# Kernel tuning notes

Hardware: AMD Instinct MI355X
Metric: run time of the kernel (lower is better)

## Reference

```python
import jax, jax.numpy as jnp
import numpy as np
from jax import lax

V, B, T, H = 8000, 64, 128, 512
EMB_INIT = 0.5 / 128.0  # init_width = 0.5 / embedding_size


def setup_inputs() -> dict:
    key = jax.random.key(0)
    ks = jax.random.split(key, 9)
    return {
        "input_data": jax.random.randint(ks[0], (B, T), 0, V, dtype=jnp.int64),
        "targets": jax.random.randint(ks[1], (B, T), 0, V, dtype=jnp.int64),
        "embedding": jax.random.uniform(ks[2], (V, H), minval=-EMB_INIT, maxval=EMB_INIT, dtype=jnp.float32),
        "W1": jax.random.normal(ks[3], (2 * H, 4 * H), dtype=jnp.float32) * 0.02,
        "b1": jnp.zeros((4 * H,), dtype=jnp.float32),
        "W2": jax.random.normal(ks[4], (2 * H, 4 * H), dtype=jnp.float32) * 0.02,
        "b2": jnp.zeros((4 * H,), dtype=jnp.float32),
        "softmax_w": jax.random.normal(ks[5], (H, V), dtype=jnp.float32) * 0.02,
        "softmax_b": jnp.zeros((V,), dtype=jnp.float32),
    }


def _lstm_step(c, h, x, W, b):
    # BasicLSTMCell with forget_bias=0.0, gate order i, j, f, o
    gates = jnp.concatenate([x, h], axis=-1) @ W + b  # [B, 4H]
    i, j, f, o = jnp.split(gates, 4, axis=-1)
    c_new = c * jax.nn.sigmoid(f) + jax.nn.sigmoid(i) * jnp.tanh(j)
    h_new = jnp.tanh(c_new) * jax.nn.sigmoid(o)
    return c_new, h_new


def reference(input_data, targets, embedding, W1, b1, W2, b2, softmax_w, softmax_b):
    x = embedding[input_data]            # [B, T, H] embedding lookup
    xt = jnp.transpose(x, (1, 0, 2))     # [T, B, H] time-major for scan

    def step(carry, x_t):
        c1, h1, c2, h2 = carry
        c1, h1 = _lstm_step(c1, h1, x_t, W1, b1)
        c2, h2 = _lstm_step(c2, h2, h1, W2, b2)
        return (c1, h1, c2, h2), h2

    init = tuple(jnp.zeros((B, H), dtype=x.dtype) for _ in range(4))
    _, hs = lax.scan(step, init, xt)     # [T, B, H]

    outputs = jnp.transpose(hs, (1, 0, 2)).reshape(-1, H)  # [B*T, H]
    logits = outputs @ softmax_w + softmax_b               # [B*T, V]
    labels = targets.reshape(-1)                            # [B*T]

    logp = jax.nn.log_softmax(logits, axis=-1)
    loss = -jnp.take_along_axis(logp, labels[:, None], axis=1)[:, 0]  # per-token CE
    cost = jnp.sum(loss) / (B * T)
    return cost
```

## Files before the change

kernel.cpp:

```cpp
#include <hip/hip_runtime.h>
#include <hip/hip_bf16.h>


#define V_SIZE 8000
#define VPAD   8192
#define B_SIZE 64
#define T_SIZE 128
#define H_SIZE 512
#define NG     (4 * H_SIZE)
#define HB     (H_SIZE * B_SIZE)
#define RBLK   64
#define RTH    256
#define SENT   0x7FFF7FFFu

typedef __attribute__((ext_vector_type(8))) short bf16x8;
typedef __attribute__((ext_vector_type(8))) unsigned short u16x8;
typedef __attribute__((ext_vector_type(4))) float f32x4;

__device__ __forceinline__ float bf2f(unsigned short u) {
  union { unsigned int i; float f; } x; x.i = ((unsigned int)u) << 16; return x.f;
}
__device__ __forceinline__ unsigned short f2bf(float f) {
  union { float f; unsigned int i; } x; x.f = f;
  unsigned int r = x.i + 0x7fffu + ((x.i >> 16) & 1u);
  return (unsigned short)(r >> 16);
}
__device__ __forceinline__ float sigf(float v) { return 1.f / (1.f + __expf(-v)); }
__device__ __forceinline__ float tanhf_fast(float v) {
  return 1.f - 2.f / (__expf(2.f * v) + 1.f);
}

__device__ __forceinline__ bf16x8 aload16(const unsigned short* p) {
  unsigned long long lo = __hip_atomic_load((const unsigned long long*)p,
                                            __ATOMIC_RELAXED, __HIP_MEMORY_SCOPE_AGENT);
  unsigned long long hi = __hip_atomic_load((const unsigned long long*)(p + 4),
                                            __ATOMIC_RELAXED, __HIP_MEMORY_SCOPE_AGENT);
  union { unsigned long long v[2]; bf16x8 b; } u;
  u.v[0] = lo; u.v[1] = hi;
  return u.b;
}
__device__ __forceinline__ unsigned has_sent(bf16x8 v) {
  union { bf16x8 b; unsigned u[4]; } x; x.b = v;
  return (unsigned)((x.u[0] == SENT) | (x.u[1] == SENT) |
                    (x.u[2] == SENT) | (x.u[3] == SENT));
}

__device__ __forceinline__ void load8_mall(bf16x8* d, const unsigned short* base) {
  asm volatile(
      "global_load_dwordx4 %0, %8, off sc0 sc1\n\t"
      "global_load_dwordx4 %1, %8, off offset:64 sc0 sc1\n\t"
      "global_load_dwordx4 %2, %8, off offset:128 sc0 sc1\n\t"
      "global_load_dwordx4 %3, %8, off offset:192 sc0 sc1\n\t"
      "global_load_dwordx4 %4, %8, off offset:256 sc0 sc1\n\t"
      "global_load_dwordx4 %5, %8, off offset:320 sc0 sc1\n\t"
      "global_load_dwordx4 %6, %8, off offset:384 sc0 sc1\n\t"
      "global_load_dwordx4 %7, %8, off offset:448 sc0 sc1\n\t"
      "s_waitcnt vmcnt(0)"
      : "=v"(d[0]), "=v"(d[1]), "=v"(d[2]), "=v"(d[3]),
        "=v"(d[4]), "=v"(d[5]), "=v"(d[6]), "=v"(d[7])
      : "v"(base)
      : "memory");
}

__global__ void fill_k(unsigned* __restrict__ p, unsigned v, int n) {
  int i = blockIdx.x * 256 + threadIdx.x;
  if (i < n) p[i] = v;
}

__global__ void bvp_k(const float* __restrict__ bv, float* __restrict__ bvp) {
  int i = blockIdx.x * 256 + threadIdx.x;
  bvp[i] = (i < V_SIZE) ? bv[i] : -1e30f;
}

__global__ __launch_bounds__(256) void xgather_k(const int* __restrict__ ids,
                                                 const float* __restrict__ emb,
                                                 unsigned short* __restrict__ xb) {
  int g = blockIdx.x * 256 + threadIdx.x;
  int r = g >> 6, c = g & 63;
  int t = r >> 6, b = r & 63;
  int id = ids[(size_t)b * T_SIZE + t];
  const float4* s4 = reinterpret_cast<const float4*>(emb + (size_t)id * H_SIZE + c * 8);
  float4 v0 = s4[0], v1 = s4[1];
  u16x8 o;
  o[0] = f2bf(v0.x); o[1] = f2bf(v0.y); o[2] = f2bf(v0.z); o[3] = f2bf(v0.w);
  o[4] = f2bf(v1.x); o[5] = f2bf(v1.y); o[6] = f2bf(v1.z); o[7] = f2bf(v1.w);
  *reinterpret_cast<u16x8*>(xb + (size_t)r * H_SIZE + c * 8) = o;
}

__global__ __launch_bounds__(256) void trans_k(const float* __restrict__ src,
                                               unsigned short* __restrict__ dst,
                                               int src_ld, int n_tiles, int Nsrc) {
  __shared__ float tile[64][65];
  const int tid = threadIdx.x;
  const int kt = blockIdx.x / n_tiles, nt = blockIdx.x % n_tiles;
#pragma unroll
  for (int q = 0; q < 16; ++q) {
    int f = tid + 256 * q;
    int r = f >> 6, c = f & 63;
    int col = nt * 64 + c;
    tile[r][c] = (col < Nsrc) ? src[(size_t)(kt * 64 + r) * src_ld + col] : 0.f;
  }
  __syncthreads();
#pragma unroll
  for (int q = 0; q < 2; ++q) {
    int u = tid + 256 * q;
    int n = u >> 3, kg = u & 7;
    u16x8 o;
#pragma unroll
    for (int e = 0; e < 8; ++e) o[e] = f2bf(tile[kg * 8 + e][n]);
    *reinterpret_cast<u16x8*>(dst + (size_t)(nt * 64 + n) * 512 + kt * 64 + kg * 8) = o;
  }
}

__device__ __forceinline__ void loadB8(bf16x8* p, const unsigned short* Wb,
                                       int vc, int kh, int kof) {
#pragma unroll
  for (int ks = 0; ks < 8; ++ks)
    p[ks] = *reinterpret_cast<const bf16x8*>(
        Wb + (size_t)vc * 512 + (kh * 8 + ks) * 32 + kof);
}

__global__ __launch_bounds__(RTH, 1) void recur_k(
    const float* __restrict__ W1, const float* __restrict__ W2,
    const float* __restrict__ b1, const float* __restrict__ b2,
    const unsigned short* __restrict__ xb,
    const unsigned short* __restrict__ hzero,
    unsigned short* __restrict__ h1all, unsigned short* __restrict__ h2all)
{
  __shared__ short wldsX[2 * 16 * 64 * 8];
  __shared__ short wlds1[2 * 16 * 64 * 8];
  __shared__ short wlds2[2 * 32 * 64 * 8];
  __shared__ float gbA[64][32];
  __shared__ float gbB[64][32];

  const int tid = threadIdx.x;
  const int bid = blockIdx.x;
  const int h0  = bid * 8;
  const int w   = tid >> 6, l = tid & 63;

  {
    for (int idx = tid; idx < 2 * 16 * 64; idx += RTH) {
      int ln2 = idx & 63;
      int ks  = (idx >> 6) % 16;
      int ng  = (idx >> 6) / 16;
      int n   = ln2 & 15;
      int col = (n & 3) * H_SIZE + h0 + ng * 4 + (n >> 2);
      int kb  = ks * 32 + (ln2 >> 4) * 8;
      short* dX = &wldsX[((size_t)(ng * 16 + ks) * 64 + ln2) * 8];
      short* d1 = &wlds1[((size_t)(ng * 16 + ks) * 64 + ln2) * 8];
#pragma unroll
      for (int e = 0; e < 8; ++e) {
        dX[e] = (short)f2bf(W1[(size_t)(kb + e) * NG + col]);
        d1[e] = (short)f2bf(W1[(size_t)(H_SIZE + kb + e) * NG + col]);
      }
    }
    for (int idx = tid; idx < 2 * 32 * 64; idx += RTH) {
      int ln2 = idx & 63;
      int ks  = (idx >> 6) % 32;
      int ng  = (idx >> 6) / 32;
      int n   = ln2 & 15;
      int col = (n & 3) * H_SIZE + h0 + ng * 4 + (n >> 2);
      int kb  = ks * 32 + (ln2 >> 4) * 8;
      short* dst = &wlds2[((size_t)(ng * 32 + ks) * 64 + ln2) * 8];
#pragma unroll
      for (int e = 0; e < 8; ++e)
        dst[e] = (short)f2bf(W2[(size_t)(kb + e) * NG + col]);
    }
  }

  const int pb = tid >> 2, pq = tid & 3;
  float c1[2] = {0.f, 0.f}, c2[2] = {0.f, 0.f};
  float bias1[2][4], bias2[2][4];
#pragma unroll
  for (int hh = 0; hh < 2; ++hh)
#pragma unroll
    for (int g = 0; g < 4; ++g) {
      bias1[hh][g] = b1[g * H_SIZE + h0 + 2 * pq + hh];
      bias2[hh][g] = b2[g * H_SIZE + h0 + 2 * pq + hh];
    }
  __syncthreads();

  const int arow = w * 16 + (l & 15);
  const int kof  = (l >> 4) * 8;

  for (int t = 0; t <= T_SIZE; ++t) {
    f32x4 acc0 = {0.f, 0.f, 0.f, 0.f};
    f32x4 acc1 = {0.f, 0.f, 0.f, 0.f};
    if (t < T_SIZE) {
      const unsigned short* xr = xb + ((size_t)t * 64 + arow) * H_SIZE + kof;
#pragma unroll
      for (int ks = 0; ks < 16; ++ks) {
        bf16x8 avx = *reinterpret_cast<const bf16x8*>(xr + ks * 32);
        bf16x8 bv0 = *reinterpret_cast<const bf16x8*>(&wldsX[((size_t)(0 * 16 + ks) * 64 + l) * 8]);
        bf16x8 bv1 = *reinterpret_cast<const bf16x8*>(&wldsX[((size_t)(1 * 16 + ks) * 64 + l) * 8]);
        acc0 = __builtin_amdgcn_mfma_f32_16x16x32_bf16(avx, bv0, acc0, 0, 0, 0);
        acc1 = __builtin_amdgcn_mfma_f32_16x16x32_bf16(avx, bv1, acc1, 0, 0, 0);
      }
    }

    const unsigned short* h1src = ((t == 0) ? hzero : h1all + (size_t)(t - 1) * HB)
                                  + (size_t)arow * H_SIZE + kof;
    const unsigned short* h2src = ((t < 2) ? hzero : h2all + (size_t)(t - 2) * HB)
                                  + (size_t)arow * H_SIZE + kof;
    bf16x8 av1[16], av2[16];
    load8_mall(av1, h1src);
    load8_mall(av1 + 8, h1src + 256);
    load8_mall(av2, h2src);
    load8_mall(av2 + 8, h2src + 256);
    {
      unsigned p1m = 0, p2m = 0;
#pragma unroll
      for (int ks = 0; ks < 16; ++ks) {
        p1m |= has_sent(av1[ks]) << ks;
        p2m |= has_sent(av2[ks]) << ks;
      }
      while (p1m | p2m) {
        __builtin_amdgcn_s_sleep(2);
#pragma unroll
        for (int ks = 0; ks < 16; ++ks)
          if ((p1m >> ks) & 1) {
            av1[ks] = aload16(h1src + ks * 32);
            if (!has_sent(av1[ks])) p1m &= ~(1u << ks);
          }
#pragma unroll
        for (int ks = 0; ks < 16; ++ks)
          if ((p2m >> ks) & 1) {
            av2[ks] = aload16(h2src + ks * 32);
            if (!has_sent(av2[ks])) p2m &= ~(1u << ks);
          }
      }
    }

    if (t < T_SIZE) {
#pragma unroll
      for (int ks = 0; ks < 16; ++ks) {
        bf16x8 bv0 = *reinterpret_cast<const bf16x8*>(&wlds1[((size_t)(0 * 16 + ks) * 64 + l) * 8]);
        bf16x8 bv1 = *reinterpret_cast<const bf16x8*>(&wlds1[((size_t)(1 * 16 + ks) * 64 + l) * 8]);
        acc0 = __builtin_amdgcn_mfma_f32_16x16x32_bf16(av1[ks], bv0, acc0, 0, 0, 0);
        acc1 = __builtin_amdgcn_mfma_f32_16x16x32_bf16(av1[ks], bv1, acc1, 0, 0, 0);
      }
      {
        const int crow = w * 16 + ((l >> 4) << 2);
        const int ccol = l & 15;
#pragma unroll
        for (int r = 0; r < 4; ++r) {
          gbA[crow + r][ccol]      = acc0[r];
          gbA[crow + r][16 + ccol] = acc1[r];
        }
      }
      __syncthreads();
      unsigned short hbv[2];
#pragma unroll
      for (int hh = 0; hh < 2; ++hh) {
        const int hl = 2 * pq + hh;
        const int ng = hl >> 2, jj = hl & 3;
        float g[4];
#pragma unroll
        for (int gg = 0; gg < 4; ++gg)
          g[gg] = gbA[pb][ng * 16 + jj * 4 + gg] + bias1[hh][gg];
        float cn = c1[hh] * sigf(g[2]) + sigf(g[0]) * tanhf_fast(g[1]);
        float hn = tanhf_fast(cn) * sigf(g[3]);
        c1[hh] = cn;
        hbv[hh] = f2bf(hn);
      }
      unsigned pack = (unsigned)hbv[0] | ((unsigned)hbv[1] << 16);
      __hip_atomic_store((unsigned*)(h1all + (size_t)t * HB + (size_t)pb * H_SIZE
                                     + h0 + 2 * pq),
                         pack, __ATOMIC_RELAXED, __HIP_MEMORY_SCOPE_AGENT);
    }

    if (t >= 1) {
      f32x4 bcc0 = {0.f, 0.f, 0.f, 0.f};
      f32x4 bcc1 = {0.f, 0.f, 0.f, 0.f};
#pragma unroll
      for (int ks = 0; ks < 16; ++ks) {
        bf16x8 bv0 = *reinterpret_cast<const bf16x8*>(&wlds2[((size_t)(0 * 32 + 16 + ks) * 64 + l) * 8]);
        bf16x8 bv1 = *reinterpret_cast<const bf16x8*>(&wlds2[((size_t)(1 * 32 + 16 + ks) * 64 + l) * 8]);
        bcc0 = __builtin_amdgcn_mfma_f32_16x16x32_bf16(av2[ks], bv0, bcc0, 0, 0, 0);
        bcc1 = __builtin_amdgcn_mfma_f32_16x16x32_bf16(av2[ks], bv1, bcc1, 0, 0, 0);
      }
#pragma unroll
      for (int ks = 0; ks < 16; ++ks) {
        bf16x8 bv0 = *reinterpret_cast<const bf16x8*>(&wlds2[((size_t)(0 * 32 + ks) * 64 + l) * 8]);
        bf16x8 bv1 = *reinterpret_cast<const bf16x8*>(&wlds2[((size_t)(1 * 32 + ks) * 64 + l) * 8]);
        bcc0 = __builtin_amdgcn_mfma_f32_16x16x32_bf16(av1[ks], bv0, bcc0, 0, 0, 0);
        bcc1 = __builtin_amdgcn_mfma_f32_16x16x32_bf16(av1[ks], bv1, bcc1, 0, 0, 0);
      }
      {
        const int crow = w * 16 + ((l >> 4) << 2);
        const int ccol = l & 15;
#pragma unroll
        for (int r = 0; r < 4; ++r) {
          gbB[crow + r][ccol]      = bcc0[r];
          gbB[crow + r][16 + ccol] = bcc1[r];
        }
      }
      __syncthreads();
      unsigned short hbv[2];
#pragma unroll
      for (int hh = 0; hh < 2; ++hh) {
        const int hl = 2 * pq + hh;
        const int ng = hl >> 2, jj = hl & 3;
        float g[4];
#pragma unroll
        for (int gg = 0; gg < 4; ++gg)
          g[gg] = gbB[pb][ng * 16 + jj * 4 + gg] + bias2[hh][gg];
        float cn = c2[hh] * sigf(g[2]) + sigf(g[0]) * tanhf_fast(g[1]);
        float hn = tanhf_fast(cn) * sigf(g[3]);
        c2[hh] = cn;
        hbv[hh] = f2bf(hn);
      }
      unsigned pack = (unsigned)hbv[0] | ((unsigned)hbv[1] << 16);
      __hip_atomic_store((unsigned*)(h2all + (size_t)(t - 1) * HB
                                     + (size_t)pb * H_SIZE + h0 + 2 * pq),
                         pack, __ATOMIC_RELAXED, __HIP_MEMORY_SCOPE_AGENT);
    }

    __syncthreads();
  }
}

__global__ __launch_bounds__(512) void ce2_k(const unsigned short* __restrict__ outs,
                                             const unsigned short* __restrict__ Wvb,
                                             const float* __restrict__ bvp,
                                             const int* __restrict__ tgts,
                                             float* __restrict__ psm,
                                             float* __restrict__ ptg) {
  const int tid = threadIdx.x;
  const int rb = blockIdx.x >> 3, cb = blockIdx.x & 7;
  const int w = tid >> 6, l = tid & 63;
  const int kof = (l >> 4) * 8;
  const int ln = l & 15;
  const int r0 = rb * 256 + w * 32;
  const int cbase = cb * 1024;

  bf16x8 av0[16], av1[16];
#pragma unroll
  for (int ks = 0; ks < 16; ++ks) {
    av0[ks] = *reinterpret_cast<const bf16x8*>(
        outs + (size_t)(r0 + ln) * H_SIZE + ks * 32 + kof);
    av1[ks] = *reinterpret_cast<const bf16x8*>(
        outs + (size_t)(r0 + 16 + ln) * H_SIZE + ks * 32 + kof);
  }
  int lbl0[4], lbl1[4];
#pragma unroll
  for (int r = 0; r < 4; ++r) {
    int rr = r0 + ((l >> 4) << 2) + r;
    lbl0[r] = tgts[(size_t)(rr & 63) * T_SIZE + (rr >> 6)];
    rr += 16;
    lbl1[r] = tgts[(size_t)(rr & 63) * T_SIZE + (rr >> 6)];
  }

  float sm0[4] = {0.f, 0.f, 0.f, 0.f}, sm1[4] = {0.f, 0.f, 0.f, 0.f};
  float tg0[4] = {0.f, 0.f, 0.f, 0.f}, tg1[4] = {0.f, 0.f, 0.f, 0.f};

  bf16x8 p0[8], p1[8];
  loadB8(p0, Wvb, cbase + ln, 0, kof);
  for (int ct = 0; ct < 64; ++ct) {
    const int vc = cbase + ct * 16 + ln;
    const int vcn = cbase + ((ct < 63) ? ct + 1 : ct) * 16 + ln;
    f32x4 a0 = {0.f, 0.f, 0.f, 0.f};
    f32x4 a1 = {0.f, 0.f, 0.f, 0.f};
    loadB8(p1, Wvb, vc, 1, kof);
#pragma unroll
    for (int ks = 0; ks < 8; ++ks) {
      a0 = __builtin_amdgcn_mfma_f32_16x16x32_bf16(av0[ks], p0[ks], a0, 0, 0, 0);
      a1 = __builtin_amdgcn_mfma_f32_16x16x32_bf16(av1[ks], p0[ks], a1, 0, 0, 0);
    }
    loadB8(p0, Wvb, vcn, 0, kof);
#pragma unroll
    for (int ks = 0; ks < 8; ++ks) {
      a0 = __builtin_amdgcn_mfma_f32_16x16x32_bf16(av0[8 + ks], p1[ks], a0, 0, 0, 0);
      a1 = __builtin_amdgcn_mfma_f32_16x16x32_bf16(av1[8 + ks], p1[ks], a1, 0, 0, 0);
    }
    float bb = bvp[vc];
#pragma unroll
    for (int r = 0; r < 4; ++r) {
      float lg = a0[r] + bb;
      sm0[r] += __expf(lg);
      tg0[r] += (vc == lbl0[r]) ? lg : 0.f;
      float lh = a1[r] + bb;
      sm1[r] += __expf(lh);
      tg1[r] += (vc == lbl1[r]) ? lh : 0.f;
    }
  }

#pragma unroll
  for (int off = 1; off <= 8; off <<= 1) {
#pragma unroll
    for (int r = 0; r < 4; ++r) {
      sm0[r] += __shfl_xor(sm0[r], off, 64);
      tg0[r] += __shfl_xor(tg0[r], off, 64);
      sm1[r] += __shfl_xor(sm1[r], off, 64);
      tg1[r] += __shfl_xor(tg1[r], off, 64);
    }
  }
  if (ln == 0) {
    int rrw = r0 + ((l >> 4) << 2);
#pragma unroll
    for (int r = 0; r < 4; ++r) {
      psm[(size_t)cb * 8192 + rrw + r]      = sm0[r];
      ptg[(size_t)cb * 8192 + rrw + r]      = tg0[r];
      psm[(size_t)cb * 8192 + rrw + 16 + r] = sm1[r];
      ptg[(size_t)cb * 8192 + rrw + 16 + r] = tg1[r];
    }
  }
}

__global__ __launch_bounds__(256) void cemerge_k(const float* __restrict__ psm,
                                                 const float* __restrict__ ptg,
                                                 float* __restrict__ accum) {
  int g = blockIdx.x * 256 + threadIdx.x;
  float S = 0.f, T = 0.f;
#pragma unroll
  for (int j = 0; j < 8; ++j) {
    S += psm[(size_t)j * 8192 + g];
    T += ptg[(size_t)j * 8192 + g];
  }
  float loss = logf(S) - T;
#pragma unroll
  for (int off = 32; off >= 1; off >>= 1)
    loss += __shfl_xor(loss, off, 64);
  if ((threadIdx.x & 63) == 0) atomicAdd(accum, loss);
}

__global__ void finish_k(const float* __restrict__ accum, float* __restrict__ out) {
  out[0] = accum[0] * (1.f / (float)(B_SIZE * T_SIZE));
}

extern "C" void kernel_launch(void* const* d_in, const int* in_sizes, int n_in,
                              void* d_out, int out_size, void* d_ws, size_t ws_size,
                              hipStream_t stream) {
  const int*   ids  = (const int*)  d_in[0];
  const int*   tgts = (const int*)  d_in[1];
  const float* emb  = (const float*)d_in[2];
  const float* W1   = (const float*)d_in[3];
  const float* b1   = (const float*)d_in[4];
  const float* W2   = (const float*)d_in[5];
  const float* b2   = (const float*)d_in[6];
  const float* Wv   = (const float*)d_in[7];
  const float* bv   = (const float*)d_in[8];
  float* out = (float*)d_out;

  char* ws = (char*)d_ws;
  unsigned short* xb    = (unsigned short*)(ws);
  unsigned short* outsb = (unsigned short*)(ws + 8388608);
  unsigned short* h1all = (unsigned short*)(ws + 16777216);
  unsigned short* Wvb   = (unsigned short*)(ws + 25165824);
  unsigned short* hzero = (unsigned short*)(ws + 33554432);
  float*          bvp   = (float*)         (ws + 33619968);
  float*          accum = (float*)         (ws + 33652736);
  float*          psm   = (float*)         (ws + 33652800);
  float*          ptg   = (float*)         (ws + 33914944);

  fill_k<<<97, 256, 0, stream>>>((unsigned*)hzero, 0u, 24592);
  fill_k<<<16384, 256, 0, stream>>>((unsigned*)outsb, SENT, 4194304);

  bvp_k<<<32, 256, 0, stream>>>(bv, bvp);
  xgather_k<<<2048, 256, 0, stream>>>(ids, emb, xb);
  trans_k<<<1024, 256, 0, stream>>>(Wv, Wvb, V_SIZE, 128, V_SIZE);

  {
    void* args[] = { (void*)&W1, (void*)&W2, (void*)&b1, (void*)&b2,
                     (void*)&xb, (void*)&hzero, (void*)&h1all, (void*)&outsb };
    hipError_t e = hipLaunchCooperativeKernel((const void*)recur_k,
                                              dim3(RBLK), dim3(RTH),
                                              args, 0, stream);
    if (e != hipSuccess) {
      recur_k<<<dim3(RBLK), dim3(RTH), 0, stream>>>(W1, W2, b1, b2, xb, hzero,
                                                    h1all, outsb);
    }
  }

  ce2_k<<<256, 512, 0, stream>>>(outsb, Wvb, bvp, tgts, psm, ptg);
  cemerge_k<<<32, 256, 0, stream>>>(psm, ptg, accum);
  finish_k<<<1, 1, 0, stream>>>(accum, out);
}
```

Baseline: 1.524 ms.

## Compute LSTM gates in-register via lane shuffles instead of LDS round-trip

```diff
diff --git a/kernel.cpp b/kernel.cpp
--- a/kernel.cpp
+++ b/kernel.cpp
@@ -107,7 +107,10 @@
     int n = u >> 3, kg = u & 7;
     u16x8 o;
 #pragma unroll
-    for (int e = 0; e < 8; ++e) o[e] = f2bf(tile[kg * 8 + e][n]);
+    for (int e = 0; e < 8; ++e) {
+      int cm = (e >> 1) + 4 * (e & 1);
+      o[e] = f2bf(tile[kg * 8 + cm][n]);
+    }
     *reinterpret_cast<u16x8*>(dst + (size_t)(nt * 64 + n) * 512 + kt * 64 + kg * 8) = o;
   }
 }
@@ -122,7 +125,7 @@
 
 __global__ __launch_bounds__(RTH, 1) void recur_k(
     const float* __restrict__ W1, const float* __restrict__ W2,
-    const float* __restrict__ b1, const float* __restrict__ b2,
+    const float* __restrict__ b1f, const float* __restrict__ b2f,
     const unsigned short* __restrict__ xb,
     const unsigned short* __restrict__ hzero,
     unsigned short* __restrict__ h1all, unsigned short* __restrict__ h2all)
@@ -130,13 +133,13 @@
   __shared__ short wldsX[2 * 16 * 64 * 8];
   __shared__ short wlds1[2 * 16 * 64 * 8];
   __shared__ short wlds2[2 * 32 * 64 * 8];
-  __shared__ float gbA[64][32];
-  __shared__ float gbB[64][32];
 
   const int tid = threadIdx.x;
   const int bid = blockIdx.x;
   const int h0  = bid * 8;
   const int w   = tid >> 6, l = tid & 63;
+  const int q   = (l >> 2) & 3;
+  const bool leader = (l & 3) == 0;
 
   {
     for (int idx = tid; idx < 2 * 16 * 64; idx += RTH) {
@@ -150,8 +153,9 @@
       short* d1 = &wlds1[((size_t)(ng * 16 + ks) * 64 + ln2) * 8];
 #pragma unroll
       for (int e = 0; e < 8; ++e) {
+        int cm = (e >> 1) + 4 * (e & 1);
         dX[e] = (short)f2bf(W1[(size_t)(kb + e) * NG + col]);
-        d1[e] = (short)f2bf(W1[(size_t)(H_SIZE + kb + e) * NG + col]);
+        d1[e] = (short)f2bf(W1[(size_t)(H_SIZE + kb + cm) * NG + col]);
       }
     }
     for (int idx = tid; idx < 2 * 32 * 64; idx += RTH) {
@@ -163,21 +167,23 @@
       int kb  = ks * 32 + (ln2 >> 4) * 8;
       short* dst = &wlds2[((size_t)(ng * 32 + ks) * 64 + ln2) * 8];
 #pragma unroll
-      for (int e = 0; e < 8; ++e)
-        dst[e] = (short)f2bf(W2[(size_t)(kb + e) * NG + col]);
-    }
-  }
-
-  const int pb = tid >> 2, pq = tid & 3;
-  float c1[2] = {0.f, 0.f}, c2[2] = {0.f, 0.f};
-  float bias1[2][4], bias2[2][4];
-#pragma unroll
-  for (int hh = 0; hh < 2; ++hh)
-#pragma unroll
-    for (int g = 0; g < 4; ++g) {
-      bias1[hh][g] = b1[g * H_SIZE + h0 + 2 * pq + hh];
-      bias2[hh][g] = b2[g * H_SIZE + h0 + 2 * pq + hh];
-    }
+      for (int e = 0; e < 8; ++e) {
+        int cm = (e >> 1) + 4 * (e & 1);
+        dst[e] = (short)f2bf(W2[(size_t)(kb + cm) * NG + col]);
+      }
+    }
+  }
+
+  float bA1[4], bB1[4], bA2[4], bB2[4];
+#pragma unroll
+  for (int g = 0; g < 4; ++g) {
+    bA1[g] = b1f[g * H_SIZE + h0 + q];
+    bB1[g] = b1f[g * H_SIZE + h0 + q + 4];
+    bA2[g] = b2f[g * H_SIZE + h0 + q];
+    bB2[g] = b2f[g * H_SIZE + h0 + q + 4];
+  }
+  float c1a[4] = {0,0,0,0}, c1b[4] = {0,0,0,0};
+  float c2a[4] = {0,0,0,0}, c2b[4] = {0,0,0,0};
   __syncthreads();
 
   const int arow = w * 16 + (l & 15);
@@ -239,34 +245,37 @@
         acc0 = __builtin_amdgcn_mfma_f32_16x16x32_bf16(av1[ks], bv0, acc0, 0, 0, 0);
         acc1 = __builtin_amdgcn_mfma_f32_16x16x32_bf16(av1[ks], bv1, acc1, 0, 0, 0);
       }
-      {
-        const int crow = w * 16 + ((l >> 4) << 2);
-        const int ccol = l & 15;
+      unsigned pk[4];
+#pragma unroll
+      for (int r = 0; r < 4; ++r) {
+        float aj = __shfl_xor(acc0[r], 1, 64);
+        float af = __shfl_xor(acc0[r], 2, 64);
+        float ao = __shfl_xor(acc0[r], 3, 64);
+        float bj = __shfl_xor(acc1[r], 1, 64);
+        float bfv = __shfl_xor(acc1[r], 2, 64);
+        float bo = __shfl_xor(acc1[r], 3, 64);
+        float ia = sigf(acc0[r] + bA1[0]);
+        float ja = tanhf_fast(aj + bA1[1]);
+        float fa = sigf(af + bA1[2]);
+        float oa = sigf(ao + bA1[3]);
+        float cna = c1a[r] * fa + ia * ja; c1a[r] = cna;
+        float ha = tanhf_fast(cna) * oa;
+        float ib = sigf(acc1[r] + bB1[0]);
+        float jb = tanhf_fast(bj + bB1[1]);
+        float fb = sigf(bfv + bB1[2]);
+        float ob = sigf(bo + bB1[3]);
+        float cnb = c1b[r] * fb + ib * jb; c1b[r] = cnb;
+        float hb = tanhf_fast(cnb) * ob;
+        pk[r] = (unsigned)f2bf(ha) | ((unsigned)f2bf(hb) << 16);
+      }
+      if (leader) {
 #pragma unroll
         for (int r = 0; r < 4; ++r) {
-          gbA[crow + r][ccol]      = acc0[r];
-          gbA[crow + r][16 + ccol] = acc1[r];
+          unsigned* dst = (unsigned*)(h1all + (size_t)t * HB
+                          + (size_t)(w * 16 + (l >> 4) * 4 + r) * H_SIZE + h0 + 2 * q);
+          __hip_atomic_store(dst, pk[r], __ATOMIC_RELAXED, __HIP_MEMORY_SCOPE_AGENT);
         }
       }
-      __syncthreads();
-      unsigned short hbv[2];
-#pragma unroll
-      for (int hh = 0; hh < 2; ++hh) {
-        const int hl = 2 * pq + hh;
-        const int ng = hl >> 2, jj = hl & 3;
-        float g[4];
-#pragma unroll
-        for (int gg = 0; gg < 4; ++gg)
-          g[gg] = gbA[pb][ng * 16 + jj * 4 + gg] + bias1[hh][gg];
-        float cn = c1[hh] * sigf(g[2]) + sigf(g[0]) * tanhf_fast(g[1]);
-        float hn = tanhf_fast(cn) * sigf(g[3]);
-        c1[hh] = cn;
-        hbv[hh] = f2bf(hn);
-      }
-      unsigned pack = (unsigned)hbv[0] | ((unsigned)hbv[1] << 16);
-      __hip_atomic_store((unsigned*)(h1all + (size_t)t * HB + (size_t)pb * H_SIZE
-                                     + h0 + 2 * pq),
-                         pack, __ATOMIC_RELAXED, __HIP_MEMORY_SCOPE_AGENT);
     }
 
     if (t >= 1) {
@@ -286,37 +295,38 @@
         bcc0 = __builtin_amdgcn_mfma_f32_16x16x32_bf16(av1[ks], bv0, bcc0, 0, 0, 0);
         bcc1 = __builtin_amdgcn_mfma_f32_16x16x32_bf16(av1[ks], bv1, bcc1, 0, 0, 0);
       }
-      {
-        const int crow = w * 16 + ((l >> 4) << 2);
-        const int ccol = l & 15;
+      unsigned pk[4];
+#pragma unroll
+      for (int r = 0; r < 4; ++r) {
+        float aj = __shfl_xor(bcc0[r], 1, 64);
+        float af = __shfl_xor(bcc0[r], 2, 64);
+        float ao = __shfl_xor(bcc0[r], 3, 64);
+        float bj = __shfl_xor(bcc1[r], 1, 64);
+        float bfv = __shfl_xor(bcc1[r], 2, 64);
+        float bo = __shfl_xor(bcc1[r], 3, 64);
+        float ia = sigf(bcc0[r] + bA2[0]);
+        float ja = tanhf_fast(aj + bA2[1]);
+        float fa = sigf(af + bA2[2]);
+        float oa = sigf(ao + bA2[3]);
+        float cna = c2a[r] * fa + ia * ja; c2a[r] = cna;
+        float ha = tanhf_fast(cna) * oa;
+        float ib = sigf(bcc1[r] + bB2[0]);
+        float jb = tanhf_fast(bj + bB2[1]);
+        float fb = sigf(bfv + bB2[2]);
+        float ob = sigf(bo + bB2[3]);
+        float cnb = c2b[r] * fb + ib * jb; c2b[r] = cnb;
+        float hb = tanhf_fast(cnb) * ob;
+        pk[r] = (unsigned)f2bf(ha) | ((unsigned)f2bf(hb) << 16);
+      }
+      if (leader) {
 #pragma unroll
         for (int r = 0; r < 4; ++r) {
-          gbB[crow + r][ccol]      = bcc0[r];
-          gbB[crow + r][16 + ccol] = bcc1[r];
+          unsigned* dst = (unsigned*)(h2all + (size_t)(t - 1) * HB
+                          + (size_t)(w * 16 + (l >> 4) * 4 + r) * H_SIZE + h0 + 2 * q);
+          __hip_atomic_store(dst, pk[r], __ATOMIC_RELAXED, __HIP_MEMORY_SCOPE_AGENT);
         }
       }
-      __syncthreads();
-      unsigned short hbv[2];
-#pragma unroll
-      for (int hh = 0; hh < 2; ++hh) {
-        const int hl = 2 * pq + hh;
-        const int ng = hl >> 2, jj = hl & 3;
-        float g[4];
-#pragma unroll
-        for (int gg = 0; gg < 4; ++gg)
-          g[gg] = gbB[pb][ng * 16 + jj * 4 + gg] + bias2[hh][gg];
-        float cn = c2[hh] * sigf(g[2]) + sigf(g[0]) * tanhf_fast(g[1]);
-        float hn = tanhf_fast(cn) * sigf(g[3]);
-        c2[hh] = cn;
-        hbv[hh] = f2bf(hn);
-      }
-      unsigned pack = (unsigned)hbv[0] | ((unsigned)hbv[1] << 16);
-      __hip_atomic_store((unsigned*)(h2all + (size_t)(t - 1) * HB
-                                     + (size_t)pb * H_SIZE + h0 + 2 * pq),
-                         pack, __ATOMIC_RELAXED, __HIP_MEMORY_SCOPE_AGENT);
-    }
-
-    __syncthreads();
+    }
   }
 }
 
```

Result: slower. 1.683 ms (+10.4%).
